# Optimization experiments

Hardware: AMD Instinct MI355X
Metric: run time of the kernel (lower is better)

Reference implementation:

```python
import math
import jax, jax.numpy as jnp
import numpy as np

B, S, H, NH, BS, R = 2, 4096, 1024, 16, 64, 3
HD = H // NH          # 64 head dim
L = S // BS           # 64 blocks
PEN = -10000.0


def _make_rand_attn():
    # data-independent random block plan (like HF bigbird, seeded numpy),
    # per head, per middle query block: R random key blocks excluding
    # global blocks (0, L-1) and the sliding window (i-1, i, i+1)
    rng = np.random.RandomState(42)
    ra = np.zeros((NH, L - 2, R), dtype=np.int64)
    for h in range(NH):
        for i in range(1, L - 1):
            choices = np.array([j for j in range(L) if j not in (0, i - 1, i, i + 1, L - 1)])
            ra[h, i - 1] = rng.choice(choices, R, replace=False)
    return ra


def setup_inputs():
    key = jax.random.key(0)
    ks = jax.random.split(key, 8)
    sc = 1.0 / math.sqrt(H)
    return {
        "Q": jax.random.normal(ks[0], (B, S, H), jnp.float32),
        "K": jax.random.normal(ks[1], (B, S, H), jnp.float32),
        "V": jax.random.normal(ks[2], (B, S, H), jnp.float32),
        "mask": jnp.ones((B, S), jnp.float32),
        "Wq": jax.random.normal(ks[3], (H, H), jnp.float32) * sc,
        "bq": jnp.zeros((H,), jnp.float32),
        "Wk": jax.random.normal(ks[4], (H, H), jnp.float32) * sc,
        "bk": jnp.zeros((H,), jnp.float32),
        "Wv": jax.random.normal(ks[5], (H, H), jnp.float32) * sc,
        "bv": jnp.zeros((H,), jnp.float32),
        "rand_attn": jnp.asarray(_make_rand_attn()),
    }


def _forward(Q, K, V, mask, Wq, bq, Wk, bk, Wv, bv, rand_attn):
    rsd = 1.0 / math.sqrt(HD)
    sm = lambda x: jax.nn.softmax(x, axis=-1)

    def proj(x, W, b):  # torch Linear: x @ W^T + b, then split heads
        return (x @ W.T + b).reshape(B, S, NH, HD).transpose(0, 2, 1, 3)

    q = proj(Q, Wq, bq)  # [B,NH,S,HD]
    k = proj(K, Wk, bk)
    v = proj(V, Wv, bv)
    qb = q.reshape(B, NH, L, BS, HD)
    kb = k.reshape(B, NH, L, BS, HD)
    vb = v.reshape(B, NH, L, BS, HD)

    # ---- masks (derived from padding mask, as in HF create_masks_...) ----
    blocked = mask.reshape(B, L, BS)
    from_mask = mask[:, None, :, None]   # [B,1,S,1]
    to_mask = mask[:, None, None, :]     # [B,1,1,S]
    exp_to = jnp.concatenate([blocked[:, 1:-3], blocked[:, 2:-2], blocked[:, 3:-1]], axis=2)  # [B,L-4,3BS]
    band_mask = jnp.einsum('blq,blk->blqk', blocked[:, 2:-2], exp_to)[:, None]  # [B,1,L-4,BS,3BS]

    ra = jnp.broadcast_to(rand_attn[None], (B, NH, L - 2, R))
    bidx = jnp.arange(B)[:, None, None, None]
    hidx = jnp.arange(NH)[None, :, None, None]
    gk = kb[bidx, hidx, ra].reshape(B, NH, L - 2, R * BS, HD)  # gathered random key blocks
    gv = vb[bidx, hidx, ra].reshape(B, NH, L - 2, R * BS, HD)
    rm = blocked[bidx, ra].reshape(B, NH, L - 2, R * BS)
    rand_mask = jnp.einsum('blq,bhlk->bhlqk', blocked[:, 1:-1], rm)  # [B,NH,L-2,BS,R*BS]

    # ---- first block: dense attention over all keys ----
    p1 = jnp.einsum('bhqd,bhkd->bhqk', qb[:, :, 0], k) * rsd + (1.0 - to_mask) * PEN
    ctx_first = jnp.einsum('bhqk,bhkd->bhqd', sm(p1), v)

    # ---- second block: global(0) + window(1,2) + last + random ----
    k2 = jnp.concatenate([kb[:, :, 0], kb[:, :, 1], kb[:, :, 2], kb[:, :, -1], gk[:, :, 0]], axis=2)
    v2 = jnp.concatenate([vb[:, :, 0], vb[:, :, 1], vb[:, :, 2], vb[:, :, -1], gv[:, :, 0]], axis=2)
    p2 = jnp.einsum('bhqd,bhkd->bhqk', qb[:, :, 1], k2) * rsd
    seq_pad2 = jnp.concatenate([to_mask[..., :3 * BS], to_mask[..., -BS:],
                                jnp.ones((B, 1, 1, R * BS), mask.dtype)], axis=3)
    rand_pad2 = jnp.concatenate([jnp.ones((B, NH, BS, 4 * BS), mask.dtype), rand_mask[:, :, 0]], axis=3)
    p2 = p2 + (1.0 - jnp.minimum(seq_pad2, rand_pad2)) * PEN
    ctx_second = jnp.einsum('bhqk,bhkd->bhqd', sm(p2), v2)

    # ---- middle blocks: band (3 sliding) + random + 2 global ----
    exp_k = jnp.concatenate([kb[:, :, 1:-3], kb[:, :, 2:-2], kb[:, :, 3:-1]], axis=3)  # [B,NH,L-4,3BS,HD]
    exp_v = jnp.concatenate([vb[:, :, 1:-3], vb[:, :, 2:-2], vb[:, :, 3:-1]], axis=3)
    mq = qb[:, :, 2:-2]
    inner = jnp.einsum('bhlqd,bhlkd->bhlqk', mq, exp_k) * rsd + (1.0 - band_mask) * PEN
    randp = jnp.einsum('bhlqd,bhlkd->bhlqk', mq, gk[:, :, 1:-1]) * rsd + (1.0 - rand_mask[:, :, 1:-1]) * PEN
    firstp = jnp.einsum('bhlqd,bhkd->bhlqk', mq, kb[:, :, 0]) * rsd + (1.0 - to_mask[:, :, :, None, :BS]) * PEN
    lastp = jnp.einsum('bhlqd,bhkd->bhlqk', mq, kb[:, :, -1]) * rsd + (1.0 - to_mask[:, :, :, None, -BS:]) * PEN
    w = sm(jnp.concatenate([firstp, inner, randp, lastp], axis=-1))  # [B,NH,L-4,BS,(5+R)*BS]
    ctx_mid = jnp.einsum('bhlqk,bhlkd->bhlqd', w[..., BS:4 * BS], exp_v)
    ctx_mid += jnp.einsum('bhlqk,bhlkd->bhlqd', w[..., 4 * BS:(4 + R) * BS], gv[:, :, 1:-1])
    ctx_mid += jnp.einsum('bhlqk,bhkd->bhlqd', w[..., :BS], vb[:, :, 0])
    ctx_mid += jnp.einsum('bhlqk,bhkd->bhlqd', w[..., -BS:], vb[:, :, -1])

    # ---- second-to-last block ----
    k3 = jnp.concatenate([kb[:, :, 0], kb[:, :, -3], kb[:, :, -2], kb[:, :, -1], gk[:, :, -1]], axis=2)
    v3 = jnp.concatenate([vb[:, :, 0], vb[:, :, -3], vb[:, :, -2], vb[:, :, -1], gv[:, :, -1]], axis=2)
    p3 = jnp.einsum('bhqd,bhkd->bhqk', qb[:, :, -2], k3) * rsd
    seq_pad3 = jnp.concatenate([to_mask[..., :BS], to_mask[..., -3 * BS:],
                                jnp.ones((B, 1, 1, R * BS), mask.dtype)], axis=3)
    rand_pad3 = jnp.concatenate([jnp.ones((B, NH, BS, 4 * BS), mask.dtype), rand_mask[:, :, -1]], axis=3)
    p3 = p3 + (1.0 - jnp.minimum(seq_pad3, rand_pad3)) * PEN
    ctx_seclast = jnp.einsum('bhqk,bhkd->bhqd', sm(p3), v3)

    # ---- last block: dense attention over all keys ----
    p4 = jnp.einsum('bhqd,bhkd->bhqk', qb[:, :, -1], k) * rsd + (1.0 - to_mask) * PEN
    ctx_last = jnp.einsum('bhqk,bhkd->bhqd', sm(p4), v)

    ctx = jnp.concatenate([ctx_first[:, :, None], ctx_second[:, :, None], ctx_mid,
                           ctx_seclast[:, :, None], ctx_last[:, :, None]], axis=2)
    ctx = ctx.reshape(B, NH, S, HD) * from_mask
    return ctx.transpose(0, 2, 1, 3).reshape(B, S, NH * HD)


def reference(Q, K, V, mask, Wq, bq, Wk, bk, Wv, bv, rand_attn):
    return _forward(Q, K, V, mask, Wq, bq, Wk, bk, Wv, bv, rand_attn)
```

## Files before the change

kernel.cpp:

```cpp
#include <hip/hip_runtime.h>
#include <hip/hip_bf16.h>
#include <stdint.h>

#define BB 2
#define SS 4096
#define HH 1024
#define NHh 16
#define HD 64
#define LL 64
#define BS 64
#define RR 3
#define PENf (-10000.0f)

typedef unsigned int uint;
typedef __attribute__((ext_vector_type(8))) short bf16x8;
typedef __attribute__((ext_vector_type(4))) float f32x4;

__device__ __forceinline__ ushort f2bf(float f) {
    union { float f; uint u; } v; v.f = f;
    uint u = v.u;
    return (ushort)((u + 0x7fffu + ((u >> 16) & 1u)) >> 16);
}
__device__ __forceinline__ uint pack_bf(float a, float b) {
    return (uint)f2bf(a) | (((uint)f2bf(b)) << 16);
}
__device__ __forceinline__ uint scale_pair(uint w) {
    float lo = __uint_as_float(w << 16) * 0.125f;
    float hi = __uint_as_float(w & 0xffff0000u) * 0.125f;
    return (uint)f2bf(lo) | (((uint)f2bf(hi)) << 16);
}
__device__ __forceinline__ uint4 scale4(uint4 w) {
    uint4 o;
    o.x = scale_pair(w.x); o.y = scale_pair(w.y);
    o.z = scale_pair(w.z); o.w = scale_pair(w.w);
    return o;
}
__device__ __forceinline__ void async16(const ushort* g, ushort* l) {
    __builtin_amdgcn_global_load_lds((const __attribute__((address_space(1))) uint*)g,
                                     (__attribute__((address_space(3))) uint*)l,
                                     16, 0, 0);
}

__global__ __launch_bounds__(256)
void cvt_kernel(const float* __restrict__ Xq, const float* __restrict__ Xk,
                const float* __restrict__ Xv, const float* __restrict__ Wq,
                const float* __restrict__ Wk, const float* __restrict__ Wv,
                ushort* __restrict__ Xbf, ushort* __restrict__ Wbf)
{
    const size_t XTOT = (size_t)3 * BB * SS * HH;
    const size_t UNITS = (XTOT + (size_t)3 * HH * HH) / 8;
    for (size_t u = (size_t)blockIdx.x * 256 + threadIdx.x; u < UNITS;
         u += (size_t)gridDim.x * 256) {
        const size_t e = u * 8;
        const float* src; ushort* dst;
        if (e < XTOT) {
            const int zz = (int)(e >> 23);
            src = (zz == 0 ? Xq : zz == 1 ? Xk : Xv) + (e & ((1u << 23) - 1));
            dst = Xbf + e;
        } else {
            const size_t e2 = e - XTOT;
            const int zz = (int)(e2 >> 20);
            src = (zz == 0 ? Wq : zz == 1 ? Wk : Wv) + (e2 & ((1u << 20) - 1));
            dst = Wbf + e2;
        }
        float4 a = ((const float4*)src)[0];
        float4 c = ((const float4*)src)[1];
        uint4 o;
        o.x = pack_bf(a.x, a.y); o.y = pack_bf(a.z, a.w);
        o.z = pack_bf(c.x, c.y); o.w = pack_bf(c.z, c.w);
        *(uint4*)dst = o;
    }
}

__global__ __launch_bounds__(256)
void gemm3_kernel(const ushort* __restrict__ Xbf, const ushort* __restrict__ Wbf,
                  const float* __restrict__ bq, const float* __restrict__ bk,
                  const float* __restrict__ bv,
                  ushort* __restrict__ qb, ushort* __restrict__ kb,
                  ushort* __restrict__ vbT)
{
    __shared__ __align__(16) ushort smem[128 * 136];
    ushort* As = smem;
    ushort* Bs = smem + 4096;

    const int z = blockIdx.z;
    const ushort* A  = Xbf + (size_t)z * ((size_t)BB * SS * HH);
    const ushort* Bt = Wbf + (size_t)z * (HH * HH);
    const float* bias = (z == 0) ? bq : (z == 1) ? bk : bv;

    const int tid = threadIdx.x;
    const int m0 = blockIdx.x * 128;
    const int n0 = blockIdx.y * 128;
    const int wave = tid >> 6;
    const int lane = tid & 63;
    const int l15 = lane & 15;
    const int quad = lane >> 4;
    const int wr = wave >> 1, wc = wave & 1;

    f32x4 acc[4][4];
#pragma unroll
    for (int mt = 0; mt < 4; ++mt)
#pragma unroll
        for (int nt = 0; nt < 4; ++nt) acc[mt][nt] = (f32x4){0.f, 0.f, 0.f, 0.f};

    const int r0 = wave * 32 + (lane >> 2);
    const int p8 = (lane & 3) * 8;
    const ushort* Abase = A + (size_t)(m0 + r0) * HH + p8;
    const ushort* Bbase = Bt + (size_t)(n0 + r0) * HH + p8;
    ushort* ldsA0 = As + wave * 1024;
    ushort* ldsA1 = As + wave * 1024 + 512;
    ushort* ldsB0 = Bs + wave * 1024;
    ushort* ldsB1 = Bs + wave * 1024 + 512;

    for (int k0 = 0; k0 < HH; k0 += 32) {
        async16(Abase + k0, ldsA0);
        async16(Abase + 16 * HH + k0, ldsA1);
        async16(Bbase + k0, ldsB0);
        async16(Bbase + 16 * HH + k0, ldsB1);
        __syncthreads();
        bf16x8 af[4], bfr[4];
#pragma unroll
        for (int mt = 0; mt < 4; ++mt)
            af[mt] = *(const bf16x8*)(As + (wr * 64 + mt * 16 + l15) * 32 + quad * 8);
#pragma unroll
        for (int nt = 0; nt < 4; ++nt)
            bfr[nt] = *(const bf16x8*)(Bs + (wc * 64 + nt * 16 + l15) * 32 + quad * 8);
#pragma unroll
        for (int mt = 0; mt < 4; ++mt)
#pragma unroll
            for (int nt = 0; nt < 4; ++nt)
                acc[mt][nt] = __builtin_amdgcn_mfma_f32_16x16x32_bf16(af[mt], bfr[nt], acc[mt][nt], 0, 0, 0);
        __syncthreads();
    }

    if (z < 2) {
        ushort* outp = (z == 0) ? qb : kb;
#pragma unroll
        for (int nt = 0; nt < 4; ++nt) {
            const int n = n0 + wc * 64 + nt * 16 + l15;
            const float bn = bias[n];
            const int nh = n >> 6, hd = n & 63;
#pragma unroll
            for (int mt = 0; mt < 4; ++mt) {
#pragma unroll
                for (int rr = 0; rr < 4; ++rr) {
                    const int m = m0 + wr * 64 + mt * 16 + quad * 4 + rr;
                    const int bgl = m >> 12, s = m & 4095;
                    outp[((size_t)((bgl << 4) | nh) * SS + s) * HD + hd] = f2bf(acc[mt][nt][rr] + bn);
                }
            }
        }
    } else {
        __syncthreads();
        ushort* stg = smem;
#pragma unroll
        for (int nt = 0; nt < 4; ++nt) {
            const int n_local = wc * 64 + nt * 16 + l15;
            const float bn = bias[n0 + n_local];
#pragma unroll
            for (int mt = 0; mt < 4; ++mt) {
                const int m_base = wr * 64 + mt * 16 + quad * 4;
                uint2 pk;
                pk.x = pack_bf(acc[mt][nt][0] + bn, acc[mt][nt][1] + bn);
                pk.y = pack_bf(acc[mt][nt][2] + bn, acc[mt][nt][3] + bn);
                *(uint2*)(stg + n_local * 136 + m_base) = pk;
            }
        }
        __syncthreads();
        const int n_row = tid >> 1;
        const int half = tid & 1;
        const int n = n0 + n_row;
        const int nh = n >> 6, hd = n & 63;
        const int bgl = m0 >> 12;
        const int sbase = (m0 & 4095) + half * 64;
        const uint4* src = (const uint4*)(stg + n_row * 136 + half * 64);
        uint4* dst = (uint4*)(vbT + ((size_t)((bgl << 4) | nh) * HD + hd) * SS + sbase);
#pragma unroll
        for (int j = 0; j < 8; ++j) dst[j] = src[j];
    }
}

__global__ __launch_bounds__(256)
void proj3_kernel(const float* __restrict__ Xq, const float* __restrict__ Xk,
                  const float* __restrict__ Xv,
                  const float* __restrict__ Wq, const float* __restrict__ Wk,
                  const float* __restrict__ Wv,
                  const float* __restrict__ bq, const float* __restrict__ bk,
                  const float* __restrict__ bv,
                  ushort* __restrict__ qb, ushort* __restrict__ kb,
                  ushort* __restrict__ vbT)
{
    __shared__ __align__(16) ushort smem[128 * 136];
    ushort* As = smem;
    ushort* Bs = smem + 128 * 40;

    const int z = blockIdx.z;
    const float* X    = (z == 0) ? Xq : (z == 1) ? Xk : Xv;
    const float* W    = (z == 0) ? Wq : (z == 1) ? Wk : Wv;
    const float* bias = (z == 0) ? bq : (z == 1) ? bk : bv;

    const int tid = threadIdx.x;
    const int m0 = blockIdx.x * 128;
    const int n0 = blockIdx.y * 128;
    const int wave = tid >> 6;
    const int lane = tid & 63;
    const int l15 = lane & 15;
    const int quad = lane >> 4;
    const int wr = wave >> 1, wc = wave & 1;

    f32x4 acc[4][4];
#pragma unroll
    for (int mt = 0; mt < 4; ++mt)
#pragma unroll
        for (int nt = 0; nt < 4; ++nt) acc[mt][nt] = (f32x4){0.f, 0.f, 0.f, 0.f};

    const int srow = tid >> 1;
    const int shalf = tid & 1;
    const float* xp = X + (size_t)(m0 + srow) * HH + shalf * 16;
    const float* wp = W + (size_t)(n0 + srow) * HH + shalf * 16;
    ushort* asw = As + srow * 40 + shalf * 16;
    ushort* bsw = Bs + srow * 40 + shalf * 16;

    for (int k0 = 0; k0 < HH; k0 += 32) {
        float4 a0 = *(const float4*)(xp + k0);
        float4 a1 = *(const float4*)(xp + k0 + 4);
        float4 a2 = *(const float4*)(xp + k0 + 8);
        float4 a3 = *(const float4*)(xp + k0 + 12);
        float4 b0 = *(const float4*)(wp + k0);
        float4 b1 = *(const float4*)(wp + k0 + 4);
        float4 b2 = *(const float4*)(wp + k0 + 8);
        float4 b3 = *(const float4*)(wp + k0 + 12);
        __syncthreads();
        uint4 pa, pb;
        pa.x = pack_bf(a0.x, a0.y); pa.y = pack_bf(a0.z, a0.w);
        pa.z = pack_bf(a1.x, a1.y); pa.w = pack_bf(a1.z, a1.w);
        *(uint4*)asw = pa;
        pa.x = pack_bf(a2.x, a2.y); pa.y = pack_bf(a2.z, a2.w);
        pa.z = pack_bf(a3.x, a3.y); pa.w = pack_bf(a3.z, a3.w);
        *(uint4*)(asw + 8) = pa;
        pb.x = pack_bf(b0.x, b0.y); pb.y = pack_bf(b0.z, b0.w);
        pb.z = pack_bf(b1.x, b1.y); pb.w = pack_bf(b1.z, b1.w);
        *(uint4*)bsw = pb;
        pb.x = pack_bf(b2.x, b2.y); pb.y = pack_bf(b2.z, b2.w);
        pb.z = pack_bf(b3.x, b3.y); pb.w = pack_bf(b3.z, b3.w);
        *(uint4*)(bsw + 8) = pb;
        __syncthreads();

        bf16x8 af[4], bfr[4];
#pragma unroll
        for (int mt = 0; mt < 4; ++mt)
            af[mt] = *(const bf16x8*)(As + (wr * 64 + mt * 16 + l15) * 40 + quad * 8);
#pragma unroll
        for (int nt = 0; nt < 4; ++nt)
            bfr[nt] = *(const bf16x8*)(Bs + (wc * 64 + nt * 16 + l15) * 40 + quad * 8);
#pragma unroll
        for (int mt = 0; mt < 4; ++mt)
#pragma unroll
            for (int nt = 0; nt < 4; ++nt)
                acc[mt][nt] = __builtin_amdgcn_mfma_f32_16x16x32_bf16(af[mt], bfr[nt], acc[mt][nt], 0, 0, 0);
    }

    if (z < 2) {
        ushort* outp = (z == 0) ? qb : kb;
#pragma unroll
        for (int nt = 0; nt < 4; ++nt) {
            const int n = n0 + wc * 64 + nt * 16 + l15;
            const float bn = bias[n];
            const int nh = n >> 6, hd = n & 63;
#pragma unroll
            for (int mt = 0; mt < 4; ++mt) {
#pragma unroll
                for (int rr = 0; rr < 4; ++rr) {
                    const int m = m0 + wr * 64 + mt * 16 + quad * 4 + rr;
                    const int bgl = m >> 12, s = m & 4095;
                    outp[((size_t)((bgl << 4) | nh) * SS + s) * HD + hd] = f2bf(acc[mt][nt][rr] + bn);
                }
            }
        }
    } else {
        __syncthreads();
        ushort* stg = smem;
#pragma unroll
        for (int nt = 0; nt < 4; ++nt) {
            const int n_local = wc * 64 + nt * 16 + l15;
            const float bn = bias[n0 + n_local];
#pragma unroll
            for (int mt = 0; mt < 4; ++mt) {
                const int m_base = wr * 64 + mt * 16 + quad * 4;
                uint2 pk;
                pk.x = pack_bf(acc[mt][nt][0] + bn, acc[mt][nt][1] + bn);
                pk.y = pack_bf(acc[mt][nt][2] + bn, acc[mt][nt][3] + bn);
                *(uint2*)(stg + n_local * 136 + m_base) = pk;
            }
        }
        __syncthreads();
        const int n_row = tid >> 1;
        const int half = tid & 1;
        const int n = n0 + n_row;
        const int nh = n >> 6, hd = n & 63;
        const int bgl = m0 >> 12;
        const int sbase = (m0 & 4095) + half * 64;
        const uint4* src = (const uint4*)(stg + n_row * 136 + half * 64);
        uint4* dst = (uint4*)(vbT + ((size_t)((bgl << 4) | nh) * HD + hd) * SS + sbase);
#pragma unroll
        for (int j = 0; j < 8; ++j) dst[j] = src[j];
    }
}

__global__ __launch_bounds__(256)
void attn_kernel(const ushort* __restrict__ qg, const ushort* __restrict__ kg,
                 const ushort* __restrict__ vTg,
                 const float* __restrict__ mask, const int* __restrict__ rand_attn,
                 float* __restrict__ out, float* __restrict__ partO,
                 float* __restrict__ partML)
{
    __shared__ __align__(16) ushort qs[64][72];
    __shared__ __align__(16) ushort ks2[2][64][32];
    __shared__ __align__(16) ushort vs2[2][64][32];
    __shared__ __align__(16) ushort ps[64][72];
    __shared__ __align__(16) float qm_s[64];
    __shared__ __align__(16) float km_s[64];

    const int tid = threadIdx.x;
    const int wid = blockIdx.x;
    const int bh = wid / 78;
    const int r = wid - bh * 78;
    const int b = bh >> 4, h = bh & 15;

    int i, nkb;
    int kbl[8], pfl[8];
    bool dense;
    int part = 0, which = 0;
    if (r < 62) {
        dense = false;
        i = r + 1;
        const int* ra = rand_attn + ((size_t)h * (LL - 2) + (i - 1)) * RR;
        if (i == 1) {
            kbl[0] = 0; kbl[1] = 1; kbl[2] = 2; kbl[3] = LL - 1;
            kbl[4] = ra[0]; kbl[5] = ra[1]; kbl[6] = ra[2]; kbl[7] = 0;
            pfl[0] = pfl[1] = pfl[2] = pfl[3] = 0;
            pfl[4] = pfl[5] = pfl[6] = 1; pfl[7] = 0;
            nkb = 7;
        } else if (i == LL - 2) {
            kbl[0] = 0; kbl[1] = LL - 3; kbl[2] = LL - 2; kbl[3] = LL - 1;
            kbl[4] = ra[0]; kbl[5] = ra[1]; kbl[6] = ra[2]; kbl[7] = 0;
            pfl[0] = pfl[1] = pfl[2] = pfl[3] = 0;
            pfl[4] = pfl[5] = pfl[6] = 1; pfl[7] = 0;
            nkb = 7;
        } else {
            kbl[0] = 0;      pfl[0] = 0;
            kbl[1] = i - 1;  pfl[1] = 1;
            kbl[2] = i;      pfl[2] = 1;
            kbl[3] = i + 1;  pfl[3] = 1;
            kbl[4] = LL - 1; pfl[4] = 0;
            kbl[5] = ra[0]; kbl[6] = ra[1]; kbl[7] = ra[2];
            pfl[5] = pfl[6] = pfl[7] = 1;
            nkb = 8;
        }
    } else {
        dense = true;
        const int r2 = r - 62;
        which = r2 >> 3;
        part = r2 & 7;
        i = which ? (LL - 1) : 0;
        nkb = 8;
#pragma unroll
        for (int j = 0; j < 8; ++j) { kbl[j] = part * 8 + j; pfl[j] = 0; }
    }

    const int lane = tid & 63;
    const int wave = tid >> 6;
    const int l15 = lane & 15;
    const int quad = lane >> 4;

    {
        const int row = tid >> 2;
        const int c0 = (tid & 3) * 16;
        const ushort* src = qg + ((size_t)bh * SS + i * BS + row) * HD + c0;
        uint4 w0 = *(const uint4*)src;
        uint4 w1 = *(const uint4*)(src + 8);
        *(uint4*)&qs[row][c0] = scale4(w0);
        *(uint4*)&qs[row][c0 + 8] = scale4(w1);
        if (tid < 64) qm_s[tid] = mask[(size_t)b * SS + i * BS + tid];
    }
    __syncthreads();
    bf16x8 aq[2];
    aq[0] = *(const bf16x8*)&qs[wave * 16 + l15][quad * 8];
    aq[1] = *(const bf16x8*)&qs[wave * 16 + l15][32 + quad * 8];
    const float qm = qm_s[wave * 16 + l15];

    float mrow = -1e30f, lrow = 0.0f;
    f32x4 accO[4];
#pragma unroll
    for (int dt = 0; dt < 4; ++dt) accO[dt] = (f32x4){0.f, 0.f, 0.f, 0.f};

    const int srow = lane >> 2;
    const int p8 = (lane & 3) * 8;
    const ushort* kgb = kg + (size_t)bh * SS * HD;
    const ushort* vgb = vTg + (size_t)bh * HD * SS;

    for (int it = 0; it < nkb; ++it) {
        const int kb_ = kbl[it];
        const int pf = pfl[it];
        __syncthreads();
        {
            const size_t krow = (size_t)(kb_ * BS + wave * 16 + srow) * HD;
            async16(kgb + krow + p8,      &ks2[0][wave * 16][0]);
            async16(kgb + krow + 32 + p8, &ks2[1][wave * 16][0]);
            const size_t vrow = (size_t)(wave * 16 + srow) * SS + kb_ * BS;
            async16(vgb + vrow + p8,      &vs2[0][wave * 16][0]);
            async16(vgb + vrow + 32 + p8, &vs2[1][wave * 16][0]);
            if (tid < 64) km_s[tid] = mask[(size_t)b * SS + kb_ * BS + tid];
        }
        __syncthreads();

        f32x4 sc[4];
#pragma unroll
        for (int nt = 0; nt < 4; ++nt) sc[nt] = (f32x4){0.f, 0.f, 0.f, 0.f};
#pragma unroll
        for (int c = 0; c < 2; ++c) {
#pragma unroll
            for (int nt = 0; nt < 4; ++nt) {
                bf16x8 af = *(const bf16x8*)&ks2[c][nt * 16 + l15][quad * 8];
                sc[nt] = __builtin_amdgcn_mfma_f32_16x16x32_bf16(af, aq[c], sc[nt], 0, 0, 0);
            }
        }

        float p[4][4];
        float bm = -1e30f;
#pragma unroll
        for (int nt = 0; nt < 4; ++nt) {
            const float4 km4 = *(const float4*)&km_s[nt * 16 + quad * 4];
            const float kmv[4] = {km4.x, km4.y, km4.z, km4.w};
#pragma unroll
            for (int rr = 0; rr < 4; ++rr) {
                const float pm = pf ? (qm * kmv[rr]) : kmv[rr];
                const float sv = sc[nt][rr] + (1.0f - pm) * PENf;
                p[nt][rr] = sv;
                bm = fmaxf(bm, sv);
            }
        }
        bm = fmaxf(bm, __shfl_xor(bm, 16));
        bm = fmaxf(bm, __shfl_xor(bm, 32));
        const float mn = fmaxf(mrow, bm);
        const float alpha = __expf(mrow - mn);
        mrow = mn;
        float ls = 0.0f;
#pragma unroll
        for (int nt = 0; nt < 4; ++nt)
#pragma unroll
            for (int rr = 0; rr < 4; ++rr) {
                p[nt][rr] = __expf(p[nt][rr] - mn);
                ls += p[nt][rr];
            }
        ls += __shfl_xor(ls, 16);
        ls += __shfl_xor(ls, 32);
        lrow = lrow * alpha + ls;

#pragma unroll
        for (int nt = 0; nt < 4; ++nt) {
            uint2 pk;
            pk.x = pack_bf(p[nt][0], p[nt][1]);
            pk.y = pack_bf(p[nt][2], p[nt][3]);
            *(uint2*)&ps[wave * 16 + l15][nt * 16 + quad * 4] = pk;
        }
        float a4[4];
#pragma unroll
        for (int rr = 0; rr < 4; ++rr) a4[rr] = __shfl(alpha, quad * 4 + rr, 64);
#pragma unroll
        for (int dt = 0; dt < 4; ++dt) {
#pragma unroll
            for (int rr = 0; rr < 4; ++rr) accO[dt][rr] *= a4[rr];
        }

#pragma unroll
        for (int c = 0; c < 2; ++c) {
            bf16x8 ap = *(const bf16x8*)&ps[wave * 16 + l15][c * 32 + quad * 8];
#pragma unroll
            for (int dt = 0; dt < 4; ++dt) {
                bf16x8 bvf = *(const bf16x8*)&vs2[c][dt * 16 + l15][quad * 8];
                accO[dt] = __builtin_amdgcn_mfma_f32_16x16x32_bf16(ap, bvf, accO[dt], 0, 0, 0);
            }
        }
    }

    if (!dense) {
#pragma unroll
        for (int rr = 0; rr < 4; ++rr) {
            const int qloc = quad * 4 + rr;
            const float lq = __shfl(lrow, qloc, 64);
            const float inv = qm_s[wave * 16 + qloc] / lq;
#pragma unroll
            for (int dt = 0; dt < 4; ++dt) {
                const int d = dt * 16 + l15;
                out[((size_t)b * SS + i * BS + wave * 16 + qloc) * HH + h * HD + d] = accO[dt][rr] * inv;
            }
        }
    } else {
        const int slot = (bh * 2 + which) * 8 + part;
        float* po = partO + (size_t)slot * 4096;
#pragma unroll
        for (int rr = 0; rr < 4; ++rr) {
            const int qrow = wave * 16 + quad * 4 + rr;
#pragma unroll
            for (int dt = 0; dt < 4; ++dt) {
                const int d = dt * 16 + l15;
                po[qrow * 64 + d] = accO[dt][rr];
            }
        }
        if (lane < 16) {
            partML[slot * 128 + wave * 16 + lane] = mrow;
            partML[slot * 128 + 64 + wave * 16 + lane] = lrow;
        }
    }
}

__global__ __launch_bounds__(256)
void combine_kernel(const float* __restrict__ partO, const float* __restrict__ partML,
                    const float* __restrict__ mask, float* __restrict__ out)
{
    const int g = blockIdx.x;
    const int bh = g >> 1, which = g & 1;
    const int b = bh >> 4, h = bh & 15;
    const int i = which ? (LL - 1) : 0;
    const int t = threadIdx.x;
    const int row = t >> 2;
    const int d0 = (t & 3) * 16;
    const int base = g * 8;

    float mp[8], lp[8];
    float M = -1e30f;
#pragma unroll
    for (int p = 0; p < 8; ++p) {
        mp[p] = partML[(base + p) * 128 + row];
        lp[p] = partML[(base + p) * 128 + 64 + row];
        M = fmaxf(M, mp[p]);
    }
    float L = 0.0f, w[8];
#pragma unroll
    for (int p = 0; p < 8; ++p) { w[p] = __expf(mp[p] - M); L += lp[p] * w[p]; }

    float4 o[4];
#pragma unroll
    for (int j = 0; j < 4; ++j) o[j] = make_float4(0.f, 0.f, 0.f, 0.f);
#pragma unroll
    for (int p = 0; p < 8; ++p) {
        const float* po = partO + (size_t)(base + p) * 4096 + row * 64 + d0;
#pragma unroll
        for (int j = 0; j < 4; ++j) {
            float4 v = *(const float4*)(po + j * 4);
            o[j].x = fmaf(w[p], v.x, o[j].x);
            o[j].y = fmaf(w[p], v.y, o[j].y);
            o[j].z = fmaf(w[p], v.z, o[j].z);
            o[j].w = fmaf(w[p], v.w, o[j].w);
        }
    }
    const float fm = mask[(size_t)b * SS + i * BS + row];
    const float inv = fm / L;
    float* dst = out + ((size_t)b * SS + i * BS + row) * HH + h * HD + d0;
#pragma unroll
    for (int j = 0; j < 4; ++j) {
        float4 v;
        v.x = o[j].x * inv; v.y = o[j].y * inv;
        v.z = o[j].z * inv; v.w = o[j].w * inv;
        *(float4*)(dst + j * 4) = v;
    }
}

extern "C" void kernel_launch(void* const* d_in, const int* in_sizes, int n_in,
                              void* d_out, int out_size, void* d_ws, size_t ws_size,
                              hipStream_t stream) {
    (void)in_sizes; (void)n_in; (void)out_size;
    const float* Q    = (const float*)d_in[0];
    const float* K    = (const float*)d_in[1];
    const float* V    = (const float*)d_in[2];
    const float* mask = (const float*)d_in[3];
    const float* Wq   = (const float*)d_in[4];
    const float* bq   = (const float*)d_in[5];
    const float* Wk   = (const float*)d_in[6];
    const float* bk   = (const float*)d_in[7];
    const float* Wv   = (const float*)d_in[8];
    const float* bv   = (const float*)d_in[9];
    const int*   ra   = (const int*)d_in[10];
    float* out = (float*)d_out;

    const size_t qkv = (size_t)BB * NHh * SS * HD;
    ushort* qb  = (ushort*)d_ws;
    ushort* kb  = qb + qkv;
    ushort* vbT = kb + qkv;
    float* partO  = (float*)(vbT + qkv);
    float* partML = partO + (size_t)512 * 4096;
    ushort* Xbf = (ushort*)(partML + (size_t)512 * 128);
    ushort* Wbf = Xbf + 3 * qkv;
    const size_t need = (size_t)((char*)(Wbf + (size_t)3 * HH * HH) - (char*)d_ws);

    if (ws_size >= need) {
        cvt_kernel<<<4096, 256, 0, stream>>>(Q, K, V, Wq, Wk, Wv, Xbf, Wbf);
        gemm3_kernel<<<dim3(64, 8, 3), 256, 0, stream>>>(Xbf, Wbf, bq, bk, bv, qb, kb, vbT);
    } else {
        proj3_kernel<<<dim3(64, 8, 3), 256, 0, stream>>>(Q, K, V, Wq, Wk, Wv, bq, bk, bv,
                                                         qb, kb, vbT);
    }
    attn_kernel<<<dim3(BB * NHh * 78), 256, 0, stream>>>(qb, kb, vbT, mask, ra,
                                                         out, partO, partML);
    combine_kernel<<<dim3(BB * NHh * 2), 256, 0, stream>>>(partO, partML, mask, out);
}
```

Before: 304.5 us.

## Double-buffer GEMM and attention tile loads, vectorize QK stores, flatten convert kernel

The projection GEMM now double-buffers its async global-to-LDS tiles, so the next K-slice is fetched while the current one feeds the MFMAs. The per-step barrier count drops from two to one. For Q/K it swaps the MFMA operands so each lane holds four consecutive head-dim values, allowing packed 8-byte bf16 stores with a float4 bias load. The attention kernel prefetches the next K/V block and its key mask into a second LDS buffer, and reuses the Q staging buffer for P to offset the extra LDS. The convert kernel launches one thread per 8-element unit instead of a grid-stride loop. The cost is more LDS per block and reliance on the single barrier to order the async writes.

```diff
diff --git a/kernel.cpp b/kernel.cpp
--- a/kernel.cpp
+++ b/kernel.cpp
@@ -48,28 +48,25 @@
                 ushort* __restrict__ Xbf, ushort* __restrict__ Wbf)
 {
     const size_t XTOT = (size_t)3 * BB * SS * HH;
-    const size_t UNITS = (XTOT + (size_t)3 * HH * HH) / 8;
-    for (size_t u = (size_t)blockIdx.x * 256 + threadIdx.x; u < UNITS;
-         u += (size_t)gridDim.x * 256) {
-        const size_t e = u * 8;
-        const float* src; ushort* dst;
-        if (e < XTOT) {
-            const int zz = (int)(e >> 23);
-            src = (zz == 0 ? Xq : zz == 1 ? Xk : Xv) + (e & ((1u << 23) - 1));
-            dst = Xbf + e;
-        } else {
-            const size_t e2 = e - XTOT;
-            const int zz = (int)(e2 >> 20);
-            src = (zz == 0 ? Wq : zz == 1 ? Wk : Wv) + (e2 & ((1u << 20) - 1));
-            dst = Wbf + e2;
-        }
-        float4 a = ((const float4*)src)[0];
-        float4 c = ((const float4*)src)[1];
-        uint4 o;
-        o.x = pack_bf(a.x, a.y); o.y = pack_bf(a.z, a.w);
-        o.z = pack_bf(c.x, c.y); o.w = pack_bf(c.z, c.w);
-        *(uint4*)dst = o;
-    }
+    const uint u = blockIdx.x * 256 + threadIdx.x;
+    const size_t e = (size_t)u * 8;
+    const float* src; ushort* dst;
+    if (e < XTOT) {
+        const int zz = (int)(e >> 23);
+        src = (zz == 0 ? Xq : zz == 1 ? Xk : Xv) + (e & ((1u << 23) - 1));
+        dst = Xbf + e;
+    } else {
+        const size_t e2 = e - XTOT;
+        const int zz = (int)(e2 >> 20);
+        src = (zz == 0 ? Wq : zz == 1 ? Wk : Wv) + (e2 & ((1u << 20) - 1));
+        dst = Wbf + e2;
+    }
+    float4 a = ((const float4*)src)[0];
+    float4 c = ((const float4*)src)[1];
+    uint4 o;
+    o.x = pack_bf(a.x, a.y); o.y = pack_bf(a.z, a.w);
+    o.z = pack_bf(c.x, c.y); o.w = pack_bf(c.z, c.w);
+    *(uint4*)dst = o;
 }
 
 __global__ __launch_bounds__(256)
@@ -81,7 +78,7 @@
 {
     __shared__ __align__(16) ushort smem[128 * 136];
     ushort* As = smem;
-    ushort* Bs = smem + 4096;
+    ushort* Bs = smem + 8192;
 
     const int z = blockIdx.z;
     const ushort* A  = Xbf + (size_t)z * ((size_t)BB * SS * HH);
@@ -99,55 +96,67 @@
 
     f32x4 acc[4][4];
 #pragma unroll
-    for (int mt = 0; mt < 4; ++mt)
-#pragma unroll
-        for (int nt = 0; nt < 4; ++nt) acc[mt][nt] = (f32x4){0.f, 0.f, 0.f, 0.f};
-
-    const int r0 = wave * 32 + (lane >> 2);
+    for (int i = 0; i < 4; ++i)
+#pragma unroll
+        for (int j = 0; j < 4; ++j) acc[i][j] = (f32x4){0.f, 0.f, 0.f, 0.f};
+
     const int p8 = (lane & 3) * 8;
-    const ushort* Abase = A + (size_t)(m0 + r0) * HH + p8;
-    const ushort* Bbase = Bt + (size_t)(n0 + r0) * HH + p8;
-    ushort* ldsA0 = As + wave * 1024;
-    ushort* ldsA1 = As + wave * 1024 + 512;
-    ushort* ldsB0 = Bs + wave * 1024;
-    ushort* ldsB1 = Bs + wave * 1024 + 512;
-
-    for (int k0 = 0; k0 < HH; k0 += 32) {
-        async16(Abase + k0, ldsA0);
-        async16(Abase + 16 * HH + k0, ldsA1);
-        async16(Bbase + k0, ldsB0);
-        async16(Bbase + 16 * HH + k0, ldsB1);
+    const ushort* Abase = A + (size_t)(m0 + wave * 32 + (lane >> 2)) * HH + p8;
+    const ushort* Bbase = Bt + (size_t)(n0 + wave * 32 + (lane >> 2)) * HH + p8;
+
+#define STAGE_G(k0, bp)                                        \
+    do {                                                       \
+        ushort* A0 = As + (bp) * 4096 + wave * 1024;           \
+        ushort* B0 = Bs + (bp) * 4096 + wave * 1024;           \
+        async16(Abase + (k0), A0);                             \
+        async16(Abase + 16 * HH + (k0), A0 + 512);             \
+        async16(Bbase + (k0), B0);                             \
+        async16(Bbase + 16 * HH + (k0), B0 + 512);             \
+    } while (0)
+
+    STAGE_G(0, 0);
+    for (int k0 = 0, bp = 0; k0 < HH; k0 += 32, bp ^= 1) {
         __syncthreads();
+        if (k0 + 32 < HH) STAGE_G(k0 + 32, bp ^ 1);
         bf16x8 af[4], bfr[4];
 #pragma unroll
         for (int mt = 0; mt < 4; ++mt)
-            af[mt] = *(const bf16x8*)(As + (wr * 64 + mt * 16 + l15) * 32 + quad * 8);
+            af[mt] = *(const bf16x8*)(As + bp * 4096 + (wr * 64 + mt * 16 + l15) * 32 + quad * 8);
 #pragma unroll
         for (int nt = 0; nt < 4; ++nt)
-            bfr[nt] = *(const bf16x8*)(Bs + (wc * 64 + nt * 16 + l15) * 32 + quad * 8);
-#pragma unroll
-        for (int mt = 0; mt < 4; ++mt)
-#pragma unroll
-            for (int nt = 0; nt < 4; ++nt)
-                acc[mt][nt] = __builtin_amdgcn_mfma_f32_16x16x32_bf16(af[mt], bfr[nt], acc[mt][nt], 0, 0, 0);
-        __syncthreads();
-    }
+            bfr[nt] = *(const bf16x8*)(Bs + bp * 4096 + (wc * 64 + nt * 16 + l15) * 32 + quad * 8);
+        if (z < 2) {
+#pragma unroll
+            for (int i = 0; i < 4; ++i)
+#pragma unroll
+                for (int j = 0; j < 4; ++j)
+                    acc[i][j] = __builtin_amdgcn_mfma_f32_16x16x32_bf16(bfr[i], af[j], acc[i][j], 0, 0, 0);
+        } else {
+#pragma unroll
+            for (int i = 0; i < 4; ++i)
+#pragma unroll
+                for (int j = 0; j < 4; ++j)
+                    acc[i][j] = __builtin_amdgcn_mfma_f32_16x16x32_bf16(af[i], bfr[j], acc[i][j], 0, 0, 0);
+        }
+    }
+#undef STAGE_G
 
     if (z < 2) {
         ushort* outp = (z == 0) ? qb : kb;
 #pragma unroll
-        for (int nt = 0; nt < 4; ++nt) {
-            const int n = n0 + wc * 64 + nt * 16 + l15;
-            const float bn = bias[n];
-            const int nh = n >> 6, hd = n & 63;
-#pragma unroll
-            for (int mt = 0; mt < 4; ++mt) {
-#pragma unroll
-                for (int rr = 0; rr < 4; ++rr) {
-                    const int m = m0 + wr * 64 + mt * 16 + quad * 4 + rr;
-                    const int bgl = m >> 12, s = m & 4095;
-                    outp[((size_t)((bgl << 4) | nh) * SS + s) * HD + hd] = f2bf(acc[mt][nt][rr] + bn);
-                }
+        for (int wt = 0; wt < 4; ++wt) {
+            const int n_base = n0 + wc * 64 + wt * 16 + quad * 4;
+            const float4 b4 = *(const float4*)&bias[n_base];
+            const int nh = n_base >> 6;
+            const int hd = n_base & 63;
+#pragma unroll
+            for (int xt = 0; xt < 4; ++xt) {
+                const int m = m0 + wr * 64 + xt * 16 + l15;
+                const int bgl = m >> 12, s = m & 4095;
+                uint2 pk;
+                pk.x = pack_bf(acc[wt][xt][0] + b4.x, acc[wt][xt][1] + b4.y);
+                pk.y = pack_bf(acc[wt][xt][2] + b4.z, acc[wt][xt][3] + b4.w);
+                *(uint2*)&outp[((size_t)((bgl << 4) | nh) * SS + s) * HD + hd] = pk;
             }
         }
     } else {
@@ -314,12 +323,11 @@
                  float* __restrict__ out, float* __restrict__ partO,
                  float* __restrict__ partML)
 {
-    __shared__ __align__(16) ushort qs[64][72];
-    __shared__ __align__(16) ushort ks2[2][64][32];
-    __shared__ __align__(16) ushort vs2[2][64][32];
-    __shared__ __align__(16) ushort ps[64][72];
+    __shared__ __align__(16) ushort qs_ps[64][72];
+    __shared__ __align__(16) ushort ks2[2][2][64][32];
+    __shared__ __align__(16) ushort vs2[2][2][64][32];
     __shared__ __align__(16) float qm_s[64];
-    __shared__ __align__(16) float km_s[64];
+    __shared__ __align__(16) float km_s[2][64];
 
     const int tid = threadIdx.x;
     const int wid = blockIdx.x;
@@ -372,6 +380,20 @@
     const int wave = tid >> 6;
     const int l15 = lane & 15;
     const int quad = lane >> 4;
+    const int srow = lane >> 2;
+    const int p8 = (lane & 3) * 8;
+    const ushort* kgb = kg + (size_t)bh * SS * HD;
+    const ushort* vgb = vTg + (size_t)bh * HD * SS;
+
+#define STAGE_KV(kb_, bp)                                                        \
+    do {                                                                         \
+        const size_t krow = (size_t)((kb_) * BS + wave * 16 + srow) * HD;        \
+        async16(kgb + krow + p8,      &ks2[bp][0][wave * 16][0]);                \
+        async16(kgb + krow + 32 + p8, &ks2[bp][1][wave * 16][0]);                \
+        const size_t vrow = (size_t)(wave * 16 + srow) * SS + (kb_) * BS;        \
+        async16(vgb + vrow + p8,      &vs2[bp][0][wave * 16][0]);                \
+        async16(vgb + vrow + 32 + p8, &vs2[bp][1][wave * 16][0]);                \
+    } while (0)
 
     {
         const int row = tid >> 2;
@@ -379,14 +401,17 @@
         const ushort* src = qg + ((size_t)bh * SS + i * BS + row) * HD + c0;
         uint4 w0 = *(const uint4*)src;
         uint4 w1 = *(const uint4*)(src + 8);
-        *(uint4*)&qs[row][c0] = scale4(w0);
-        *(uint4*)&qs[row][c0 + 8] = scale4(w1);
+        *(uint4*)&qs_ps[row][c0] = scale4(w0);
+        *(uint4*)&qs_ps[row][c0 + 8] = scale4(w1);
         if (tid < 64) qm_s[tid] = mask[(size_t)b * SS + i * BS + tid];
     }
+    STAGE_KV(kbl[0], 0);
+    if (tid < 64) km_s[0][tid] = mask[(size_t)b * SS + kbl[0] * BS + tid];
     __syncthreads();
+
     bf16x8 aq[2];
-    aq[0] = *(const bf16x8*)&qs[wave * 16 + l15][quad * 8];
-    aq[1] = *(const bf16x8*)&qs[wave * 16 + l15][32 + quad * 8];
+    aq[0] = *(const bf16x8*)&qs_ps[wave * 16 + l15][quad * 8];
+    aq[1] = *(const bf16x8*)&qs_ps[wave * 16 + l15][32 + quad * 8];
     const float qm = qm_s[wave * 16 + l15];
 
     float mrow = -1e30f, lrow = 0.0f;
@@ -394,25 +419,13 @@
 #pragma unroll
     for (int dt = 0; dt < 4; ++dt) accO[dt] = (f32x4){0.f, 0.f, 0.f, 0.f};
 
-    const int srow = lane >> 2;
-    const int p8 = (lane & 3) * 8;
-    const ushort* kgb = kg + (size_t)bh * SS * HD;
-    const ushort* vgb = vTg + (size_t)bh * HD * SS;
-
     for (int it = 0; it < nkb; ++it) {
-        const int kb_ = kbl[it];
+        const int cur = it & 1;
+        if (it + 1 < nkb) {
+            STAGE_KV(kbl[it + 1], cur ^ 1);
+            if (tid < 64) km_s[cur ^ 1][tid] = mask[(size_t)b * SS + kbl[it + 1] * BS + tid];
+        }
         const int pf = pfl[it];
-        __syncthreads();
-        {
-            const size_t krow = (size_t)(kb_ * BS + wave * 16 + srow) * HD;
-            async16(kgb + krow + p8,      &ks2[0][wave * 16][0]);
-            async16(kgb + krow + 32 + p8, &ks2[1][wave * 16][0]);
-            const size_t vrow = (size_t)(wave * 16 + srow) * SS + kb_ * BS;
-            async16(vgb + vrow + p8,      &vs2[0][wave * 16][0]);
-            async16(vgb + vrow + 32 + p8, &vs2[1][wave * 16][0]);
-            if (tid < 64) km_s[tid] = mask[(size_t)b * SS + kb_ * BS + tid];
-        }
-        __syncthreads();
 
         f32x4 sc[4];
 #pragma unroll
@@ -421,7 +434,7 @@
         for (int c = 0; c < 2; ++c) {
 #pragma unroll
             for (int nt = 0; nt < 4; ++nt) {
-                bf16x8 af = *(const bf16x8*)&ks2[c][nt * 16 + l15][quad * 8];
+                bf16x8 af = *(const bf16x8*)&ks2[cur][c][nt * 16 + l15][quad * 8];
                 sc[nt] = __builtin_amdgcn_mfma_f32_16x16x32_bf16(af, aq[c], sc[nt], 0, 0, 0);
             }
         }
@@ -430,7 +443,7 @@
         float bm = -1e30f;
 #pragma unroll
         for (int nt = 0; nt < 4; ++nt) {
-            const float4 km4 = *(const float4*)&km_s[nt * 16 + quad * 4];
+            const float4 km4 = *(const float4*)&km_s[cur][nt * 16 + quad * 4];
             const float kmv[4] = {km4.x, km4.y, km4.z, km4.w};
 #pragma unroll
             for (int rr = 0; rr < 4; ++rr) {
@@ -462,7 +475,7 @@
             uint2 pk;
             pk.x = pack_bf(p[nt][0], p[nt][1]);
             pk.y = pack_bf(p[nt][2], p[nt][3]);
-            *(uint2*)&ps[wave * 16 + l15][nt * 16 + quad * 4] = pk;
+            *(uint2*)&qs_ps[wave * 16 + l15][nt * 16 + quad * 4] = pk;
         }
         float a4[4];
 #pragma unroll
@@ -475,14 +488,17 @@
 
 #pragma unroll
         for (int c = 0; c < 2; ++c) {
-            bf16x8 ap = *(const bf16x8*)&ps[wave * 16 + l15][c * 32 + quad * 8];
+            bf16x8 ap = *(const bf16x8*)&qs_ps[wave * 16 + l15][c * 32 + quad * 8];
 #pragma unroll
             for (int dt = 0; dt < 4; ++dt) {
-                bf16x8 bvf = *(const bf16x8*)&vs2[c][dt * 16 + l15][quad * 8];
+                bf16x8 bvf = *(const bf16x8*)&vs2[cur][c][dt * 16 + l15][quad * 8];
                 accO[dt] = __builtin_amdgcn_mfma_f32_16x16x32_bf16(ap, bvf, accO[dt], 0, 0, 0);
             }
         }
-    }
+
+        if (it + 1 < nkb) __syncthreads();
+    }
+#undef STAGE_KV
 
     if (!dense) {
 #pragma unroll
@@ -595,7 +611,7 @@
     const size_t need = (size_t)((char*)(Wbf + (size_t)3 * HH * HH) - (char*)d_ws);
 
     if (ws_size >= need) {
-        cvt_kernel<<<4096, 256, 0, stream>>>(Q, K, V, Wq, Wk, Wv, Xbf, Wbf);
+        cvt_kernel<<<13824, 256, 0, stream>>>(Q, K, V, Wq, Wk, Wv, Xbf, Wbf);
         gemm3_kernel<<<dim3(64, 8, 3), 256, 0, stream>>>(Xbf, Wbf, bq, bk, bv, qb, kb, vbT);
     } else {
         proj3_kernel<<<dim3(64, 8, 3), 256, 0, stream>>>(Q, K, V, Wq, Wk, Wv, bq, bk, bv,
```

Measured after the change: 303.5 us. Within noise of the previous version (-0.3%).
